# Optimization experiments

Hardware: AMD Instinct MI355X
Metric: run time of the kernel (lower is better)

Reference implementation:

```python
import jax, jax.numpy as jnp
import numpy as np
from jax import lax

B, C_IN, OUT_C, FEAT, W, HEADS, EXP = 2, 3, 12, 1024, 512, 4, 4
HEAD_DIM = FEAT // HEADS
EPS = 1e-8


def _u(key, shape, bound):
    return jax.random.uniform(key, shape, jnp.float32, -bound, bound)


def setup_inputs():
    key = jax.random.key(0)
    ks = jax.random.split(key, 16)
    fb = 1.0 / np.sqrt(FEAT)
    return {
        'x': jax.random.normal(ks[0], (B, C_IN, FEAT, W), jnp.float32),
        'embed_w': _u(ks[1], (OUT_C, C_IN, 1, 1), 1.0 / np.sqrt(C_IN)),
        'embed_b': _u(ks[2], (OUT_C,), 1.0 / np.sqrt(C_IN)),
        'ln1_w': jnp.ones((OUT_C, 1, FEAT), jnp.float32),
        'ln1_b': jnp.zeros((OUT_C, 1, FEAT), jnp.float32),
        'q_dw': _u(ks[3], (OUT_C, 1, 9, 9), 1.0 / 9.0),
        'q_pw': _u(ks[4], (OUT_C, FEAT, FEAT), fb),
        'k_dw': _u(ks[5], (OUT_C, 1, 9, 9), 1.0 / 9.0),
        'k_pw': _u(ks[6], (OUT_C, FEAT, FEAT), fb),
        'v_dw': _u(ks[7], (OUT_C, 1, 9, 9), 1.0 / 9.0),
        'v_pw': _u(ks[8], (OUT_C, FEAT, FEAT), fb),
        'o_pw': _u(ks[9], (OUT_C, FEAT, FEAT), fb),
        'ln2_w': jnp.ones((OUT_C, 1, FEAT), jnp.float32),
        'ln2_b': jnp.zeros((OUT_C, 1, FEAT), jnp.float32),
        'c1_w': _u(ks[10], (OUT_C * EXP, OUT_C, 3, 3), 1.0 / np.sqrt(OUT_C * 9)),
        'c1_b': _u(ks[11], (OUT_C * EXP,), 1.0 / np.sqrt(OUT_C * 9)),
        'c2_w': _u(ks[12], (OUT_C, OUT_C * EXP, 3, 3), 1.0 / np.sqrt(OUT_C * EXP * 9)),
        'c2_b': _u(ks[13], (OUT_C,), 1.0 / np.sqrt(OUT_C * EXP * 9)),
    }


def conv2d(x, w, b=None, pad=1, groups=1):
    y = lax.conv_general_dilated(x, w, (1, 1), [(pad, pad), (pad, pad)],
                                 dimension_numbers=('NCHW', 'OIHW', 'NCHW'),
                                 feature_group_count=groups)
    if b is not None:
        y = y + b[None, :, None, None]
    return y


def mc_layernorm(x, w, b):
    # LayerNorm over the feature (H) axis, per-channel affine. x: (b,c,h,w)
    xt = jnp.swapaxes(x, 2, 3)  # b,c,w,h
    mu = xt.mean(-1, keepdims=True)
    var = xt.var(-1, keepdims=True)
    y = (xt - mu) / jnp.sqrt(var + EPS) * w[:, 0, :][None, :, None, :] + b[:, 0, :][None, :, None, :]
    return jnp.swapaxes(y, 2, 3)


def mc_linear(x, w_pw):
    # per-channel linear over feature axis. x: (b,c,h,w), w_pw: (c,out_f,in_f)
    return jnp.einsum('bchw,cfh->bcfw', x, w_pw)


def rope(x):
    # interleaved rotary along the frame axis. x: (b,c,heads,w,d)
    d = x.shape[-1]
    inv = 1.0 / (10000.0 ** (jnp.arange(0, d, 2, dtype=jnp.float32) / d))
    t = jnp.arange(x.shape[-2], dtype=jnp.float32)
    freqs = jnp.repeat(t[:, None] * inv[None, :], 2, axis=-1)  # (w, d)
    cos, sin = jnp.cos(freqs), jnp.sin(freqs)
    xp = x.reshape(x.shape[:-1] + (d // 2, 2))
    xr = jnp.stack([-xp[..., 1], xp[..., 0]], -1).reshape(x.shape)
    return x * cos + xr * sin


def attention(x, q_dw, q_pw, k_dw, k_pw, v_dw, v_pw, o_pw):
    b, c, h, w = x.shape

    def proj(dw, pw):
        y = mc_linear(conv2d(x, dw, pad=4, groups=c), pw)  # b,c,h,w
        return jnp.swapaxes(y, 2, 3).reshape(b, c, w, HEADS, HEAD_DIM).transpose(0, 1, 3, 2, 4)

    q = rope(proj(q_dw, q_pw))
    k = rope(proj(k_dw, k_pw))
    v = proj(v_dw, v_pw)
    # NOTE: original scales by sqrt(h) = sqrt(features), not sqrt(head_dim)
    qk = jnp.einsum('bcnqd,bcnkd->bcnqk', q, k) / jnp.sqrt(jnp.float32(h))
    a = jnp.einsum('bcnqk,bcnkd->bcnqd', jax.nn.softmax(qk, -1), v)
    a = a.transpose(0, 1, 3, 2, 4).reshape(b, c, w, h)
    a = jnp.swapaxes(a, 2, 3)  # b,c,h,w
    return mc_linear(a, o_pw), qk


def _forward(x, embed_w, embed_b, ln1_w, ln1_b, q_dw, q_pw, k_dw, k_pw, v_dw, v_pw,
             o_pw, ln2_w, ln2_b, c1_w, c1_b, c2_w, c2_b):
    h = conv2d(x, embed_w, embed_b, pad=0)
    z, qk = attention(mc_layernorm(h, ln1_w, ln1_b), q_dw, q_pw, k_dw, k_pw, v_dw, v_pw, o_pw)
    h = h + z
    t = conv2d(mc_layernorm(h, ln2_w, ln2_b), c1_w, c1_b, pad=1)
    t = jnp.square(jax.nn.relu(t))
    z = conv2d(t, c2_w, c2_b, pad=1)
    h = h + z
    return jnp.concatenate((x, h), axis=1), h, qk


def reference(x, embed_w, embed_b, ln1_w, ln1_b, q_dw, q_pw, k_dw, k_pw, v_dw, v_pw,
              o_pw, ln2_w, ln2_b, c1_w, c1_b, c2_w, c2_b):
    return _forward(x, embed_w, embed_b, ln1_w, ln1_b, q_dw, q_pw, k_dw, k_pw, v_dw,
                    v_pw, o_pw, ln2_w, ln2_b, c1_w, c1_b, c2_w, c2_b)
```

## Files before the change

### kernel.cpp

```cpp
#include <hip/hip_runtime.h>
#include <math.h>

static constexpr int FEAT = 1024;
static constexpr int WDIM = 512;
static constexpr size_t PL = (size_t)FEAT * WDIM;
static constexpr size_t NB = (size_t)2 * 12 * PL;
static constexpr size_t HS = NB / 2;

typedef __attribute__((ext_vector_type(8))) short bf8_t;
typedef __attribute__((ext_vector_type(4))) float f4_t;

__device__ __forceinline__ ushort f2b(float f) {
  union { float f; unsigned u; } x; x.f = f;
  unsigned u = x.u;
  return (ushort)((u + 0x7FFFu + ((u >> 16) & 1u)) >> 16);
}

#define GLL16(g, l) __builtin_amdgcn_global_load_lds(                         \
    (const __attribute__((address_space(1))) void*)(g),                       \
    (__attribute__((address_space(3))) void*)(l), 16, 0, 0)

__global__ __launch_bounds__(256)
void k_embed(const float* __restrict__ x, const float* __restrict__ ew,
             const float* __restrict__ eb, float* __restrict__ h0)
{
  int t = blockIdx.x * 256 + threadIdx.x;
  int x4 = (t & 127) * 4;
  int y  = (t >> 7) & 1023;
  int b  = t >> 17;
  float4 xi0 = *(const float4*)&x[(((size_t)b*3+0)*FEAT + y)*WDIM + x4];
  float4 xi1 = *(const float4*)&x[(((size_t)b*3+1)*FEAT + y)*WDIM + x4];
  float4 xi2 = *(const float4*)&x[(((size_t)b*3+2)*FEAT + y)*WDIM + x4];
  #pragma unroll
  for (int c = 0; c < 12; c++) {
    float w0 = ew[c*3], w1 = ew[c*3+1], w2 = ew[c*3+2], bb = eb[c];
    float4 o;
    o.x = fmaf(xi0.x, w0, fmaf(xi1.x, w1, fmaf(xi2.x, w2, bb)));
    o.y = fmaf(xi0.y, w0, fmaf(xi1.y, w1, fmaf(xi2.y, w2, bb)));
    o.z = fmaf(xi0.z, w0, fmaf(xi1.z, w1, fmaf(xi2.z, w2, bb)));
    o.w = fmaf(xi0.w, w0, fmaf(xi1.w, w1, fmaf(xi2.w, w2, bb)));
    *(float4*)&h0[(((size_t)b*12+c)*FEAT + y)*WDIM + x4] = o;
  }
}

__global__ __launch_bounds__(256)
void k_ln(const float* __restrict__ in, const float* __restrict__ w,
          const float* __restrict__ bia, float* __restrict__ out)
{
  int bc = blockIdx.y; int c = bc % 12;
  int w0 = blockIdx.x * 64;
  int tx = threadIdx.x & 63, ty = threadIdx.x >> 6;
  const float* base = in + (size_t)bc*PL + w0;
  float s = 0.f, ss = 0.f;
  for (int h = ty; h < FEAT; h += 4) {
    float v = base[(size_t)h*WDIM + tx];
    s += v; ss = fmaf(v, v, ss);
  }
  __shared__ float S1[4][64], S2[4][64];
  S1[ty][tx] = s; S2[ty][tx] = ss;
  __syncthreads();
  if (ty == 0) {
    float t1 = S1[0][tx]+S1[1][tx]+S1[2][tx]+S1[3][tx];
    float t2 = S2[0][tx]+S2[1][tx]+S2[2][tx]+S2[3][tx];
    float mu = t1 * (1.0f/1024.0f);
    float var = t2 * (1.0f/1024.0f) - mu*mu;
    S1[0][tx] = mu; S2[0][tx] = rsqrtf(var + 1e-8f);
  }
  __syncthreads();
  float mu = S1[0][tx], ri = S2[0][tx];
  float* ob = out + (size_t)bc*PL + w0;
  for (int h = ty; h < FEAT; h += 4) {
    float v = base[(size_t)h*WDIM + tx];
    ob[(size_t)h*WDIM + tx] = (v - mu) * ri * w[c*FEAT + h] + bia[c*FEAT + h];
  }
}

__global__ __launch_bounds__(256)
void k_ln_b(const float* __restrict__ in, const float* __restrict__ w,
            const float* __restrict__ bia, ushort* __restrict__ out)
{
  int bc = blockIdx.y; int c = bc % 12;
  int w0 = blockIdx.x * 64;
  int tx = threadIdx.x & 63, ty = threadIdx.x >> 6;
  const float* base = in + (size_t)bc*PL + w0;
  float s = 0.f, ss = 0.f;
  for (int h = ty; h < FEAT; h += 4) {
    float v = base[(size_t)h*WDIM + tx];
    s += v; ss = fmaf(v, v, ss);
  }
  __shared__ float S1[4][64], S2[4][64];
  S1[ty][tx] = s; S2[ty][tx] = ss;
  __syncthreads();
  if (ty == 0) {
    float t1 = S1[0][tx]+S1[1][tx]+S1[2][tx]+S1[3][tx];
    float t2 = S2[0][tx]+S2[1][tx]+S2[2][tx]+S2[3][tx];
    float mu = t1 * (1.0f/1024.0f);
    float var = t2 * (1.0f/1024.0f) - mu*mu;
    S1[0][tx] = mu; S2[0][tx] = rsqrtf(var + 1e-8f);
  }
  __syncthreads();
  float mu = S1[0][tx], ri = S2[0][tx];
  ushort* ob = out + (size_t)bc*PL + w0;
  for (int h = ty; h < FEAT; h += 4) {
    float v = base[(size_t)h*WDIM + tx];
    ob[(size_t)h*WDIM + tx] = f2b((v - mu) * ri * w[c*FEAT + h] + bia[c*FEAT + h]);
  }
}

__global__ __launch_bounds__(256)
void k_dw3t(const float* __restrict__ in, const float* __restrict__ wq,
            const float* __restrict__ wk, const float* __restrict__ wvv,
            ushort* __restrict__ oq, ushort* __restrict__ ok2, ushort* __restrict__ ov)
{
  __shared__ float tile[72*72];
  __shared__ float wsm[3][81];
  const int bc = blockIdx.z, c = bc % 12;
  const int y0 = blockIdx.y * 64, x0 = blockIdx.x * 64;
  const int tid = threadIdx.x, lane = tid & 63, wv_ = tid >> 6;
  const float* base = in + (size_t)bc*PL;

  for (int i = tid; i < 1296; i += 256) {
    int r = i / 18, c4 = (i % 18) * 4;
    int gy = y0 - 4 + r, gx = x0 - 4 + c4;
    float4 v = {0.f,0.f,0.f,0.f};
    if ((unsigned)gy < 1024u && (unsigned)gx < 512u)
      v = *(const float4*)&base[(size_t)gy*512 + gx];
    *(float4*)&tile[r*72 + c4] = v;
  }
  if (tid < 81) { wsm[0][tid] = wq[c*81+tid]; wsm[1][tid] = wk[c*81+tid]; wsm[2][tid] = wvv[c*81+tid]; }
  __syncthreads();

  float aq[16] = {}, ak[16] = {}, av[16] = {};
  #pragma unroll 1
  for (int dx = 0; dx < 9; dx++) {
    float wq9[9], wk9[9], wv9[9];
    #pragma unroll
    for (int dy = 0; dy < 9; dy++) {
      wq9[dy] = wsm[0][dy*9+dx]; wk9[dy] = wsm[1][dy*9+dx]; wv9[dy] = wsm[2][dy*9+dx];
    }
    const float* col = &tile[(wv_*16)*72 + lane + dx];
    #pragma unroll
    for (int r = 0; r < 24; r++) {
      float v = col[r*72];
      int dylo = (r > 15) ? (r - 15) : 0;
      int dyhi = (r < 8) ? r : 8;
      #pragma unroll
      for (int dy = 0; dy < 9; dy++) {
        if (dy >= dylo && dy <= dyhi) {
          aq[r-dy] = fmaf(v, wq9[dy], aq[r-dy]);
          ak[r-dy] = fmaf(v, wk9[dy], ak[r-dy]);
          av[r-dy] = fmaf(v, wv9[dy], av[r-dy]);
        }
      }
    }
  }

  ushort* T = (ushort*)tile;
#define DW_EMIT(ACC, OUT)                                                     \
  {                                                                           \
    __syncthreads();                                                          \
    uint pk[8];                                                               \
    _Pragma("unroll")                                                         \
    for (int u = 0; u < 8; u++)                                               \
      pk[u] = (uint)f2b(ACC[2*u]) | ((uint)f2b(ACC[2*u+1]) << 16);            \
    uint4* dst = (uint4*)&T[lane*72 + wv_*16];                                \
    dst[0] = make_uint4(pk[0],pk[1],pk[2],pk[3]);                             \
    dst[1] = make_uint4(pk[4],pk[5],pk[6],pk[7]);                             \
    __syncthreads();                                                          \
    ushort* op = OUT + (size_t)bc*PL;                                         \
    _Pragma("unroll")                                                         \
    for (int it = 0; it < 2; it++) {                                          \
      int idx = it*256 + tid;                                                 \
      int xr = idx >> 3, y8 = (idx & 7) * 8;                                  \
      uint4 vv = *(uint4*)&T[xr*72 + y8];                                     \
      *(uint4*)&op[(size_t)(x0+xr)*1024 + y0 + y8] = vv;                      \
    }                                                                         \
  }
  DW_EMIT(aq, oq)
  DW_EMIT(ak, ok2)
  DW_EMIT(av, ov)
#undef DW_EMIT
}

__global__ __launch_bounds__(256)
void k_cvt4(const float* __restrict__ p0, const float* __restrict__ p1,
            const float* __restrict__ p2, const float* __restrict__ p3,
            ushort* __restrict__ out)
{
  const float* ins[4] = {p0, p1, p2, p3};
  const float* in = ins[blockIdx.y];
  size_t i = ((size_t)blockIdx.x * 256 + threadIdx.x) * 8;
  ushort* o = out + (size_t)blockIdx.y * NB + i;
  float4 v0 = *(const float4*)&in[i];
  float4 v1 = *(const float4*)&in[i+4];
  union { ushort u[8]; uint4 v; } t;
  t.u[0]=f2b(v0.x); t.u[1]=f2b(v0.y); t.u[2]=f2b(v0.z); t.u[3]=f2b(v0.w);
  t.u[4]=f2b(v1.x); t.u[5]=f2b(v1.y); t.u[6]=f2b(v1.z); t.u[7]=f2b(v1.w);
  *(uint4*)o = t.v;
}

__global__ __launch_bounds__(256)
void k_softmax(const float* __restrict__ qk, ushort* __restrict__ probs)
{
  int wave = threadIdx.x >> 6, lane = threadIdx.x & 63;
  size_t row = (size_t)blockIdx.x * 4 + wave;
  const float* r = qk + row * 512;
  float v[8];
  float m = -1e30f;
  #pragma unroll
  for (int j = 0; j < 8; j++) { v[j] = r[lane + 64*j]; m = fmaxf(m, v[j]); }
  #pragma unroll
  for (int o = 32; o; o >>= 1) m = fmaxf(m, __shfl_xor(m, o));
  float s = 0.f;
  #pragma unroll
  for (int j = 0; j < 8; j++) { v[j] = expf(v[j] - m); s += v[j]; }
  #pragma unroll
  for (int o = 32; o; o >>= 1) s += __shfl_xor(s, o);
  float inv = 1.0f / s;
  ushort* p = probs + row * 512;
  #pragma unroll
  for (int j = 0; j < 8; j++) p[lane + 64*j] = f2b(v[j] * inv);
}

template<int MODE>
__global__ __launch_bounds__(256)
void mgemm(const ushort* __restrict__ Ab, const ushort* __restrict__ Bb,
           void* __restrict__ Cb)
{
  constexpr int K   = (MODE==1) ? 256 : ((MODE==2) ? 512 : 1024);
  constexpr int LDA = (MODE==1) ? 256 : ((MODE==2) ? 512 : 1024);
  constexpr int LDB = LDA;

  const int z = blockIdx.z;
  const ushort* A; const ushort* B;
  int zz = z; size_t toff = 0;
  if constexpr (MODE==0 || MODE==4) {
    if constexpr (MODE==0) { int t = (z >= 96); zz = z - 96*t; toff = (size_t)t * NB; }
    int bc = zz >> 2, head = zz & 3, c = bc % 12;
    A = Ab + toff + ((size_t)c*1024 + head*256)*1024;
    B = Bb + toff + (size_t)bc*524288;
  } else if constexpr (MODE==1) {
    A = Ab + (size_t)z*131072; B = Bb + (size_t)z*131072;
  } else if constexpr (MODE==2) {
    A = Ab + (size_t)z*262144; B = Bb + (size_t)z*131072;
  } else {
    int c = z % 12;
    A = Ab + (size_t)c*1048576;
    B = Bb + (size_t)z*524288;
  }

  const int m0 = blockIdx.y * 128, n0 = blockIdx.x * 128;
  const int tid = threadIdx.x, lane = tid & 63, wv = tid >> 6;
  const int wr = wv >> 1, wc = wv & 1;
  const int lm = lane & 15, lg = lane >> 4;

  __shared__ __align__(16) ushort Alds[4096];
  __shared__ __align__(16) ushort Blds[4096];

  const ushort* gA0 = A + (size_t)(m0 + (2*wv)*16 + lm)*LDA + 8*lg;
  const ushort* gA1 = gA0 + (size_t)16*LDA;
  const ushort* gB0 = B + (size_t)(n0 + (2*wv)*16 + lm)*LDB + 8*lg;
  const ushort* gB1 = gB0 + (size_t)16*LDB;
  ushort* lA0 = &Alds[(2*wv)*512]; ushort* lA1 = lA0 + 512;
  ushort* lB0 = &Blds[(2*wv)*512]; ushort* lB1 = lB0 + 512;

  f4_t acc[4][4];
  #pragma unroll
  for (int i = 0; i < 4; i++)
    #pragma unroll
    for (int j = 0; j < 4; j++) acc[i][j] = (f4_t){0.f, 0.f, 0.f, 0.f};

  for (int k0 = 0; k0 < K; k0 += 32) {
    GLL16(gA0 + k0, lA0); GLL16(gA1 + k0, lA1);
    GLL16(gB0 + k0, lB0); GLL16(gB1 + k0, lB1);
    __syncthreads();
    bf8_t fa[4], fb[4];
    #pragma unroll
    for (int i = 0; i < 4; i++) fa[i] = *(const bf8_t*)&Alds[(wr*4+i)*512 + lane*8];
    #pragma unroll
    for (int j = 0; j < 4; j++) fb[j] = *(const bf8_t*)&Blds[(wc*4+j)*512 + lane*8];
    #pragma unroll
    for (int i = 0; i < 4; i++)
      #pragma unroll
      for (int j = 0; j < 4; j++)
        acc[i][j] = __builtin_amdgcn_mfma_f32_16x16x32_bf16(fa[i], fb[j], acc[i][j], 0, 0, 0);
    __syncthreads();
  }

  if constexpr (MODE==0) {
    ushort* C = (ushort*)Cb + toff + (size_t)zz*131072;
    #pragma unroll
    for (int j = 0; j < 4; j++) {
      int w = n0 + wc*64 + j*16 + lm;
      #pragma unroll
      for (int i = 0; i < 4; i++) {
        int d0 = m0 + wr*64 + i*16 + lg*4;
        int p0 = d0 >> 1;
        float inv0 = expf(-(float)p0 * 0.07195578432833848f);
        float inv1 = inv0 * 0.9305720409297794f;
        float s0, c0, s1, c1;
        sincosf((float)w * inv0, &s0, &c0);
        sincosf((float)w * inv1, &s1, &c1);
        f4_t a = acc[i][j];
        ushort4 o;
        o.x = f2b(a.x*c0 - a.y*s0);
        o.y = f2b(a.y*c0 + a.x*s0);
        o.z = f2b(a.z*c1 - a.w*s1);
        o.w = f2b(a.w*c1 + a.z*s1);
        *(ushort4*)&C[(size_t)w*256 + d0] = o;
      }
    }
  } else if constexpr (MODE==4) {
    ushort* C = (ushort*)Cb + (size_t)z*131072;
    #pragma unroll
    for (int i = 0; i < 4; i++) {
      int d0 = m0 + wr*64 + i*16 + lg*4;
      #pragma unroll
      for (int j = 0; j < 4; j++) {
        int w = n0 + wc*64 + j*16 + lm;
        f4_t a = acc[i][j];
        C[(size_t)(d0+0)*512 + w] = f2b(a.x);
        C[(size_t)(d0+1)*512 + w] = f2b(a.y);
        C[(size_t)(d0+2)*512 + w] = f2b(a.z);
        C[(size_t)(d0+3)*512 + w] = f2b(a.w);
      }
    }
  } else if constexpr (MODE==1) {
    float* C = (float*)Cb + (size_t)z*262144;
    #pragma unroll
    for (int i = 0; i < 4; i++) {
      int q0 = m0 + wr*64 + i*16 + lg*4;
      #pragma unroll
      for (int j = 0; j < 4; j++) {
        int kc = n0 + wc*64 + j*16 + lm;
        f4_t a = acc[i][j];
        C[(size_t)(q0+0)*512 + kc] = a.x * 0.03125f;
        C[(size_t)(q0+1)*512 + kc] = a.y * 0.03125f;
        C[(size_t)(q0+2)*512 + kc] = a.z * 0.03125f;
        C[(size_t)(q0+3)*512 + kc] = a.w * 0.03125f;
      }
    }
  } else if constexpr (MODE==2) {
    ushort* C = (ushort*)Cb + (size_t)(z>>2)*524288 + (size_t)(z&3)*256;
    #pragma unroll
    for (int i = 0; i < 4; i++) {
      int q0 = m0 + wr*64 + i*16 + lg*4;
      #pragma unroll
      for (int j = 0; j < 4; j++) {
        int d = n0 + wc*64 + j*16 + lm;
        f4_t a = acc[i][j];
        C[(size_t)(q0+0)*1024 + d] = f2b(a.x);
        C[(size_t)(q0+1)*1024 + d] = f2b(a.y);
        C[(size_t)(q0+2)*1024 + d] = f2b(a.z);
        C[(size_t)(q0+3)*1024 + d] = f2b(a.w);
      }
    }
  } else {
    float* C = (float*)Cb + (size_t)z*524288;
    #pragma unroll
    for (int i = 0; i < 4; i++) {
      int f0 = m0 + wr*64 + i*16 + lg*4;
      #pragma unroll
      for (int j = 0; j < 4; j++) {
        int w = n0 + wc*64 + j*16 + lm;
        f4_t a = acc[i][j];
        C[(size_t)(f0+0)*512 + w] += a.x;
        C[(size_t)(f0+1)*512 + w] += a.y;
        C[(size_t)(f0+2)*512 + w] += a.z;
        C[(size_t)(f0+3)*512 + w] += a.w;
      }
    }
  }
}

__global__ __launch_bounds__(256)
void k_pack(const float* __restrict__ c1w, const float* __restrict__ c2w,
            ushort* __restrict__ wp1, ushort* __restrict__ wp2)
{
  int tid = threadIdx.x;
  for (int i = tid; i < 48*168; i += 256) {
    int oc = i / 168, k = i % 168;
    ushort v = 0;
    if (k < 160) {
      int ofs = k >> 4, ch = k & 15;
      if (ofs < 9 && ch < 12) v = f2b(c1w[(oc*12 + ch)*9 + ofs]);
    }
    wp1[i] = v;
  }
  for (int i = tid; i < 16*584; i += 256) {
    int oc = i / 584, k = i % 584;
    ushort v = 0;
    if (k < 576) {
      int ofs = k >> 6, ch = k & 63;
      if (oc < 12 && ch < 48) v = f2b(c2w[(oc*48 + ch)*9 + ofs]);
    }
    wp2[i] = v;
  }
}

__global__ __launch_bounds__(256)
void k_c1m(const ushort* __restrict__ in, const ushort* __restrict__ Wp,
           const float* __restrict__ bias, ushort* __restrict__ out)
{
  __shared__ __align__(16) ushort Wl[48*168];
  __shared__ __align__(16) ushort Xl[4*136*16];
  __shared__ float Bs[48];
  const int b = blockIdx.z, ybase = blockIdx.y*8, x0 = blockIdx.x*128;
  const int tid = threadIdx.x, lane = tid & 63, wv = tid >> 6;
  const int lm = lane & 15, lg = lane >> 4;
  const int hl = lg >> 1, cbs = lg & 1;

  for (int i = tid; i < 48*168; i += 256) Wl[i] = Wp[i];
  for (int i = tid; i < 4*136*16; i += 256) Xl[i] = 0;
  if (tid < 48) Bs[tid] = bias[tid];

  for (int y8 = 0; y8 < 8; y8++) {
    int y = ybase + y8;
    __syncthreads();
    for (int i = tid; i < 3*34*12; i += 256) {
      int ch = i % 12, cc = (i/12) % 34, r = i/(12*34);
      int sy = y + r - 1, sx = x0 - 4 + cc*4;
      ushort4 v = (ushort4){0,0,0,0};
      if ((unsigned)sy < 1024u) {
        const ushort* p = in + ((size_t)(b*12+ch)*1024 + sy)*512 + sx;
        if (sx >= 0 && sx <= 508) v = *(const ushort4*)p;
        else {
          ushort tv[4] = {0,0,0,0};
          #pragma unroll
          for (int u = 0; u < 4; u++) { int xx = sx+u; if ((unsigned)xx < 512u) tv[u] = p[u]; }
          v = (ushort4){tv[0],tv[1],tv[2],tv[3]};
        }
      }
      int cb = ch >> 3, ce = ch & 7;
      #pragma unroll
      for (int u = 0; u < 4; u++) {
        int col = cc*4 + u;
        Xl[((r*136 + col) << 4) + ((cb ^ (col & 1)) << 3) + ce] = ((const ushort*)&v)[u];
      }
    }
    __syncthreads();

    f4_t acc[3][2];
    #pragma unroll
    for (int i = 0; i < 3; i++) { acc[i][0] = (f4_t){0,0,0,0}; acc[i][1] = (f4_t){0,0,0,0}; }
    #pragma unroll
    for (int s = 0; s < 5; s++) {
      bf8_t af[3];
      #pragma unroll
      for (int mf = 0; mf < 3; mf++)
        af[mf] = *(const bf8_t*)&Wl[(mf*16 + lm)*168 + s*32 + lg*8];
      int ofs = 2*s + hl;
      int dy = ofs / 3, dx = ofs - dy*3;
      #pragma unroll
      for (int nf = 0; nf < 2; nf++) {
        int col = (wv*2 + nf)*16 + lm + dx + 3;
        bf8_t bf = *(const bf8_t*)&Xl[((dy*136 + col) << 4) + ((cbs ^ (col & 1)) << 3)];
        #pragma unroll
        for (int mf = 0; mf < 3; mf++)
          acc[mf][nf] = __builtin_amdgcn_mfma_f32_16x16x32_bf16(af[mf], bf, acc[mf][nf], 0, 0, 0);
      }
    }
    #pragma unroll
    for (int nf = 0; nf < 2; nf++) {
      int p = (wv*2 + nf)*16 + lm;
      ushort* op = out + (((size_t)(b*1024 + y)*512) + x0 + p)*48;
      #pragma unroll
      for (int mf = 0; mf < 3; mf++) {
        int oc0 = mf*16 + lg*4;
        f4_t a = acc[mf][nf];
        float r0 = fmaxf(a.x + Bs[oc0+0], 0.f);
        float r1 = fmaxf(a.y + Bs[oc0+1], 0.f);
        float r2 = fmaxf(a.z + Bs[oc0+2], 0.f);
        float r3 = fmaxf(a.w + Bs[oc0+3], 0.f);
        ushort4 o;
        o.x = f2b(r0*r0); o.y = f2b(r1*r1); o.z = f2b(r2*r2); o.w = f2b(r3*r3);
        *(ushort4*)&op[oc0] = o;
      }
    }
  }
}

__global__ __launch_bounds__(256)
void k_c2m(const ushort* __restrict__ tin, const ushort* __restrict__ Wp,
           const float* __restrict__ bias, const float* __restrict__ h1,
           float* __restrict__ out0, float* __restrict__ out1)
{
  __shared__ __align__(16) ushort Wl[16*584];
  __shared__ __align__(16) ushort Xl[3*132*64];
  __shared__ float Bs[12];
  const int b = blockIdx.z, ybase = blockIdx.y*8, x0 = blockIdx.x*128;
  const int tid = threadIdx.x, lane = tid & 63, wv = tid >> 6;
  const int lm = lane & 15, lg = lane >> 4;

  for (int i = tid; i < 16*584; i += 256) Wl[i] = Wp[i];
  for (int i = tid; i < 3*132*64; i += 256) Xl[i] = 0;
  if (tid < 12) Bs[tid] = bias[tid];

  for (int y8 = 0; y8 < 8; y8++) {
    int y = ybase + y8;
    __syncthreads();
    for (int i = tid; i < 3*132*6; i += 256) {
      int ck = i % 6, col = (i/6) % 132, r = i/(6*132);
      int sy = y + r - 1, sx = x0 + col - 1;
      uint4 v = (uint4){0u,0u,0u,0u};
      if ((unsigned)sy < 1024u && (unsigned)sx < 512u)
        v = *(const uint4*)&tin[(((size_t)(b*1024 + sy)*512 + sx)*48) + ck*8];
      *(uint4*)&Xl[((r*132 + col) << 6) + ((ck ^ (col & 7)) << 3)] = v;
    }
    __syncthreads();

    f4_t acc[2];
    acc[0] = (f4_t){0,0,0,0}; acc[1] = (f4_t){0,0,0,0};
    #pragma unroll
    for (int s = 0; s < 18; s++) {
      bf8_t af = *(const bf8_t*)&Wl[lm*584 + s*32 + lg*8];
      int ofs = s >> 1;
      int dy = ofs / 3, dx = ofs - dy*3;
      int cb = ((s & 1) << 2) + lg;
      #pragma unroll
      for (int nf = 0; nf < 2; nf++) {
        int col = (wv*2 + nf)*16 + lm + dx;
        bf8_t bf = *(const bf8_t*)&Xl[((dy*132 + col) << 6) + ((cb ^ (col & 7)) << 3)];
        acc[nf] = __builtin_amdgcn_mfma_f32_16x16x32_bf16(af, bf, acc[nf], 0, 0, 0);
      }
    }
    if (lg < 3) {
      #pragma unroll
      for (int nf = 0; nf < 2; nf++) {
        int p = x0 + (wv*2 + nf)*16 + lm;
        f4_t a = acc[nf];
        #pragma unroll
        for (int r = 0; r < 4; r++) {
          int oc = lg*4 + r;
          size_t po = ((size_t)(b*12 + oc)*1024 + y)*512 + p;
          float hv = a[r] + Bs[oc] + h1[po];
          out1[po] = hv;
          out0[((size_t)(b*15 + 3 + oc)*1024 + y)*512 + p] = hv;
        }
      }
    }
  }
}

__global__ __launch_bounds__(256)
void k_copyx(const float* __restrict__ x, float* __restrict__ out0)
{
  int t = blockIdx.x * 256 + threadIdx.x;
  int x4 = (t & 127) * 4;
  int y  = (t >> 7) & 1023;
  int ci = (t >> 17) % 3;
  int b  = t / 393216;
  *(float4*)&out0[(((size_t)b*15 + ci)*FEAT + y)*WDIM + x4] =
      *(const float4*)&x[(((size_t)b*3 + ci)*FEAT + y)*WDIM + x4];
}

extern "C" void kernel_launch(void* const* d_in, const int* in_sizes, int n_in,
                              void* d_out, int out_size, void* d_ws, size_t ws_size,
                              hipStream_t stream)
{
  const float* x       = (const float*)d_in[0];
  const float* embed_w = (const float*)d_in[1];
  const float* embed_b = (const float*)d_in[2];
  const float* ln1_w   = (const float*)d_in[3];
  const float* ln1_b   = (const float*)d_in[4];
  const float* q_dw    = (const float*)d_in[5];
  const float* q_pw    = (const float*)d_in[6];
  const float* k_dw    = (const float*)d_in[7];
  const float* k_pw    = (const float*)d_in[8];
  const float* v_dw    = (const float*)d_in[9];
  const float* v_pw    = (const float*)d_in[10];
  const float* o_pw    = (const float*)d_in[11];
  const float* ln2_w   = (const float*)d_in[12];
  const float* ln2_b   = (const float*)d_in[13];
  const float* c1_w    = (const float*)d_in[14];
  const float* c1_b    = (const float*)d_in[15];
  const float* c2_w    = (const float*)d_in[16];
  const float* c2_b    = (const float*)d_in[17];

  float* ws = (float*)d_ws;
  float*  h0   = ws + 0*HS;
  float*  lnb  = ws + 2*HS;
  ushort* dwtq = (ushort*)(ws + 4*HS);
  ushort* dwtk = (ushort*)(ws + 5*HS);
  ushort* dwtv = (ushort*)(ws + 6*HS);
  ushort* pwbq = (ushort*)(ws + 7*HS);
  ushort* pwbo = (ushort*)(ws + 10*HS);
  ushort* Qb   = (ushort*)(ws + 11*HS);
  ushort* Vb   = (ushort*)(ws + 13*HS);
  ushort* probs= (ushort*)(ws + 4*HS);
  ushort* attt = (ushort*)(ws + 6*HS);
  ushort* Wp1  = (ushort*)(ws + 4*HS);
  ushort* Wp2  = Wp1 + 48*168;
  ushort* lnb_b= (ushort*)(ws + 2*HS);
  ushort* tcl  = (ushort*)(ws + 7*HS);

  float* out0 = (float*)d_out;
  float* out1 = out0 + (size_t)2*15*FEAT*WDIM;
  float* qk   = out1 + NB;

  k_embed<<<1024, 256, 0, stream>>>(x, embed_w, embed_b, h0);
  k_ln<<<dim3(8, 24), 256, 0, stream>>>(h0, ln1_w, ln1_b, lnb);
  k_dw3t<<<dim3(8, 16, 24), 256, 0, stream>>>(lnb, q_dw, k_dw, v_dw, dwtq, dwtk, dwtv);
  k_cvt4<<<dim3(6144, 4), 256, 0, stream>>>(q_pw, k_pw, v_pw, o_pw, pwbq);
  mgemm<0><<<dim3(4, 2, 192), 256, 0, stream>>>(pwbq, dwtq, Qb);
  mgemm<4><<<dim3(4, 2, 96), 256, 0, stream>>>((ushort*)(ws + 9*HS), dwtv, Vb);
  mgemm<1><<<dim3(4, 4, 96), 256, 0, stream>>>(Qb, (ushort*)(ws + 12*HS), qk);
  k_softmax<<<12288, 256, 0, stream>>>(qk, probs);
  mgemm<2><<<dim3(2, 4, 96), 256, 0, stream>>>(probs, Vb, attt);
  mgemm<3><<<dim3(4, 8, 24), 256, 0, stream>>>(pwbo, attt, (void*)h0);
  k_pack<<<1, 256, 0, stream>>>(c1_w, c2_w, Wp1, Wp2);
  k_ln_b<<<dim3(8, 24), 256, 0, stream>>>(h0, ln2_w, ln2_b, lnb_b);
  k_c1m<<<dim3(4, 128, 2), 256, 0, stream>>>(lnb_b, Wp1, c1_b, tcl);
  k_c2m<<<dim3(4, 128, 2), 256, 0, stream>>>(tcl, Wp2, c2_b, h0, out0, out1);
  k_copyx<<<3072, 256, 0, stream>>>(x, out0);
}
```

Baseline: 1.199 ms.

## Merge Q/K/V GEMMs, double K-step per sync, and precompute rotary table

Three changes land together. The V projection GEMM is folded into the Q/K launch as a third z-slice, giving one launch of 288 slices. The GEMM main loop now loads a 64-wide K chunk per barrier pair instead of 32, which doubles LDS use and halves the number of syncs. The rotary sin/cos factors are precomputed once into a table (stored temporarily in the qk output buffer) instead of evaluating expf and sincosf in every epilogue. The costs are higher LDS use per block, which may lower occupancy, and an extra small kernel launch.

```diff
diff --git a/kernel.cpp b/kernel.cpp
--- a/kernel.cpp
+++ b/kernel.cpp
@@ -105,6 +105,16 @@
     float v = base[(size_t)h*WDIM + tx];
     ob[(size_t)h*WDIM + tx] = f2b((v - mu) * ri * w[c*FEAT + h] + bia[c*FEAT + h]);
   }
+}
+
+__global__ __launch_bounds__(256)
+void k_rtab(float2* __restrict__ tab)
+{
+  int t = blockIdx.x * 256 + threadIdx.x;
+  int w = t >> 7, p = t & 127;
+  float ang = (float)w * expf(-(float)p * 0.07195578432833848f);
+  float s, c; sincosf(ang, &s, &c);
+  tab[t] = make_float2(c, s);
 }
 
 __global__ __launch_bounds__(256)
@@ -225,7 +235,7 @@
 template<int MODE>
 __global__ __launch_bounds__(256)
 void mgemm(const ushort* __restrict__ Ab, const ushort* __restrict__ Bb,
-           void* __restrict__ Cb)
+           void* __restrict__ Cb, const float2* __restrict__ rtab)
 {
   constexpr int K   = (MODE==1) ? 256 : ((MODE==2) ? 512 : 1024);
   constexpr int LDA = (MODE==1) ? 256 : ((MODE==2) ? 512 : 1024);
@@ -233,9 +243,9 @@
 
   const int z = blockIdx.z;
   const ushort* A; const ushort* B;
-  int zz = z; size_t toff = 0;
-  if constexpr (MODE==0 || MODE==4) {
-    if constexpr (MODE==0) { int t = (z >= 96); zz = z - 96*t; toff = (size_t)t * NB; }
+  int zz = z, t = 0; size_t toff = 0;
+  if constexpr (MODE==0) {
+    t = z / 96; zz = z - 96*t; toff = (size_t)t * NB;
     int bc = zz >> 2, head = zz & 3, c = bc % 12;
     A = Ab + toff + ((size_t)c*1024 + head*256)*1024;
     B = Bb + toff + (size_t)bc*524288;
@@ -254,15 +264,19 @@
   const int wr = wv >> 1, wc = wv & 1;
   const int lm = lane & 15, lg = lane >> 4;
 
-  __shared__ __align__(16) ushort Alds[4096];
-  __shared__ __align__(16) ushort Blds[4096];
-
-  const ushort* gA0 = A + (size_t)(m0 + (2*wv)*16 + lm)*LDA + 8*lg;
-  const ushort* gA1 = gA0 + (size_t)16*LDA;
-  const ushort* gB0 = B + (size_t)(n0 + (2*wv)*16 + lm)*LDB + 8*lg;
-  const ushort* gB1 = gB0 + (size_t)16*LDB;
-  ushort* lA0 = &Alds[(2*wv)*512]; ushort* lA1 = lA0 + 512;
-  ushort* lB0 = &Blds[(2*wv)*512]; ushort* lB1 = lB0 + 512;
+  __shared__ __align__(16) ushort Alds[8192];
+  __shared__ __align__(16) ushort Blds[8192];
+
+  const ushort* gA[4]; const ushort* gB[4];
+  ushort* lA[4]; ushort* lB[4];
+  #pragma unroll
+  for (int sl = 0; sl < 4; sl++) {
+    int mf = 2*wv + (sl >> 1), kh = sl & 1;
+    gA[sl] = A + (size_t)(m0 + mf*16 + lm)*LDA + kh*32 + 8*lg;
+    gB[sl] = B + (size_t)(n0 + mf*16 + lm)*LDB + kh*32 + 8*lg;
+    lA[sl] = &Alds[(mf*2 + kh)*512];
+    lB[sl] = &Blds[(mf*2 + kh)*512];
+  }
 
   f4_t acc[4][4];
   #pragma unroll
@@ -270,59 +284,62 @@
     #pragma unroll
     for (int j = 0; j < 4; j++) acc[i][j] = (f4_t){0.f, 0.f, 0.f, 0.f};
 
-  for (int k0 = 0; k0 < K; k0 += 32) {
-    GLL16(gA0 + k0, lA0); GLL16(gA1 + k0, lA1);
-    GLL16(gB0 + k0, lB0); GLL16(gB1 + k0, lB1);
+  for (int k0 = 0; k0 < K; k0 += 64) {
+    #pragma unroll
+    for (int sl = 0; sl < 4; sl++) { GLL16(gA[sl] + k0, lA[sl]); GLL16(gB[sl] + k0, lB[sl]); }
     __syncthreads();
-    bf8_t fa[4], fb[4];
-    #pragma unroll
-    for (int i = 0; i < 4; i++) fa[i] = *(const bf8_t*)&Alds[(wr*4+i)*512 + lane*8];
-    #pragma unroll
-    for (int j = 0; j < 4; j++) fb[j] = *(const bf8_t*)&Blds[(wc*4+j)*512 + lane*8];
-    #pragma unroll
-    for (int i = 0; i < 4; i++)
+    #pragma unroll
+    for (int kk = 0; kk < 2; kk++) {
+      bf8_t fa[4], fb[4];
+      #pragma unroll
+      for (int i = 0; i < 4; i++)
+        fa[i] = *(const bf8_t*)&Alds[(((wr*4+i)<<1) + kk)*512 + lane*8];
       #pragma unroll
       for (int j = 0; j < 4; j++)
-        acc[i][j] = __builtin_amdgcn_mfma_f32_16x16x32_bf16(fa[i], fb[j], acc[i][j], 0, 0, 0);
+        fb[j] = *(const bf8_t*)&Blds[(((wc*4+j)<<1) + kk)*512 + lane*8];
+      #pragma unroll
+      for (int i = 0; i < 4; i++)
+        #pragma unroll
+        for (int j = 0; j < 4; j++)
+          acc[i][j] = __builtin_amdgcn_mfma_f32_16x16x32_bf16(fa[i], fb[j], acc[i][j], 0, 0, 0);
+    }
     __syncthreads();
   }
 
   if constexpr (MODE==0) {
     ushort* C = (ushort*)Cb + toff + (size_t)zz*131072;
-    #pragma unroll
-    for (int j = 0; j < 4; j++) {
-      int w = n0 + wc*64 + j*16 + lm;
+    if (t < 2) {
+      #pragma unroll
+      for (int j = 0; j < 4; j++) {
+        int w = n0 + wc*64 + j*16 + lm;
+        #pragma unroll
+        for (int i = 0; i < 4; i++) {
+          int d0 = m0 + wr*64 + i*16 + lg*4;
+          int p0 = d0 >> 1;
+          float2 cs0 = rtab[w*128 + p0];
+          float2 cs1 = rtab[w*128 + p0 + 1];
+          f4_t a = acc[i][j];
+          ushort4 o;
+          o.x = f2b(a.x*cs0.x - a.y*cs0.y);
+          o.y = f2b(a.y*cs0.x + a.x*cs0.y);
+          o.z = f2b(a.z*cs1.x - a.w*cs1.y);
+          o.w = f2b(a.w*cs1.x + a.z*cs1.y);
+          *(ushort4*)&C[(size_t)w*256 + d0] = o;
+        }
+      }
+    } else {
       #pragma unroll
       for (int i = 0; i < 4; i++) {
         int d0 = m0 + wr*64 + i*16 + lg*4;
-        int p0 = d0 >> 1;
-        float inv0 = expf(-(float)p0 * 0.07195578432833848f);
-        float inv1 = inv0 * 0.9305720409297794f;
-        float s0, c0, s1, c1;
-        sincosf((float)w * inv0, &s0, &c0);
-        sincosf((float)w * inv1, &s1, &c1);
-        f4_t a = acc[i][j];
-        ushort4 o;
-        o.x = f2b(a.x*c0 - a.y*s0);
-        o.y = f2b(a.y*c0 + a.x*s0);
-        o.z = f2b(a.z*c1 - a.w*s1);
-        o.w = f2b(a.w*c1 + a.z*s1);
-        *(ushort4*)&C[(size_t)w*256 + d0] = o;
-      }
-    }
-  } else if constexpr (MODE==4) {
-    ushort* C = (ushort*)Cb + (size_t)z*131072;
-    #pragma unroll
-    for (int i = 0; i < 4; i++) {
-      int d0 = m0 + wr*64 + i*16 + lg*4;
-      #pragma unroll
-      for (int j = 0; j < 4; j++) {
-        int w = n0 + wc*64 + j*16 + lm;
-        f4_t a = acc[i][j];
-        C[(size_t)(d0+0)*512 + w] = f2b(a.x);
-        C[(size_t)(d0+1)*512 + w] = f2b(a.y);
-        C[(size_t)(d0+2)*512 + w] = f2b(a.z);
-        C[(size_t)(d0+3)*512 + w] = f2b(a.w);
+        #pragma unroll
+        for (int j = 0; j < 4; j++) {
+          int w = n0 + wc*64 + j*16 + lm;
+          f4_t a = acc[i][j];
+          C[(size_t)(d0+0)*512 + w] = f2b(a.x);
+          C[(size_t)(d0+1)*512 + w] = f2b(a.y);
+          C[(size_t)(d0+2)*512 + w] = f2b(a.z);
+          C[(size_t)(d0+3)*512 + w] = f2b(a.w);
+        }
       }
     }
   } else if constexpr (MODE==1) {
@@ -586,6 +603,7 @@
   ushort* pwbq = (ushort*)(ws + 7*HS);
   ushort* pwbo = (ushort*)(ws + 10*HS);
   ushort* Qb   = (ushort*)(ws + 11*HS);
+  ushort* Kb   = (ushort*)(ws + 12*HS);
   ushort* Vb   = (ushort*)(ws + 13*HS);
   ushort* probs= (ushort*)(ws + 4*HS);
   ushort* attt = (ushort*)(ws + 6*HS);
@@ -597,17 +615,18 @@
   float* out0 = (float*)d_out;
   float* out1 = out0 + (size_t)2*15*FEAT*WDIM;
   float* qk   = out1 + NB;
-
+  float2* rtab = (float2*)qk;
+
+  k_rtab<<<256, 256, 0, stream>>>(rtab);
   k_embed<<<1024, 256, 0, stream>>>(x, embed_w, embed_b, h0);
   k_ln<<<dim3(8, 24), 256, 0, stream>>>(h0, ln1_w, ln1_b, lnb);
   k_dw3t<<<dim3(8, 16, 24), 256, 0, stream>>>(lnb, q_dw, k_dw, v_dw, dwtq, dwtk, dwtv);
   k_cvt4<<<dim3(6144, 4), 256, 0, stream>>>(q_pw, k_pw, v_pw, o_pw, pwbq);
-  mgemm<0><<<dim3(4, 2, 192), 256, 0, stream>>>(pwbq, dwtq, Qb);
-  mgemm<4><<<dim3(4, 2, 96), 256, 0, stream>>>((ushort*)(ws + 9*HS), dwtv, Vb);
-  mgemm<1><<<dim3(4, 4, 96), 256, 0, stream>>>(Qb, (ushort*)(ws + 12*HS), qk);
+  mgemm<0><<<dim3(4, 2, 288), 256, 0, stream>>>(pwbq, dwtq, Qb, rtab);
+  mgemm<1><<<dim3(4, 4, 96), 256, 0, stream>>>(Qb, Kb, qk, nullptr);
   k_softmax<<<12288, 256, 0, stream>>>(qk, probs);
-  mgemm<2><<<dim3(2, 4, 96), 256, 0, stream>>>(probs, Vb, attt);
-  mgemm<3><<<dim3(4, 8, 24), 256, 0, stream>>>(pwbo, attt, (void*)h0);
+  mgemm<2><<<dim3(2, 4, 96), 256, 0, stream>>>(probs, Vb, attt, nullptr);
+  mgemm<3><<<dim3(4, 8, 24), 256, 0, stream>>>(pwbo, attt, (void*)h0, nullptr);
   k_pack<<<1, 256, 0, stream>>>(c1_w, c2_w, Wp1, Wp2);
   k_ln_b<<<dim3(8, 24), 256, 0, stream>>>(h0, ln2_w, ln2_b, lnb_b);
   k_c1m<<<dim3(4, 128, 2), 256, 0, stream>>>(lnb_b, Wp1, c1_b, tcl);
```

New measurement: 1.197 ms. No clear change (-0.2%).
